# Performance work log

Measured on AMD Instinct MI355X. Metric: run time of the kernel, lower is better.

The kernel has to match this reference:

```python
import jax, jax.numpy as jnp
import numpy as np

HEADS = 16

def setup_inputs() -> dict:
    key = jax.random.key(0)
    k1, k2, k3, k4 = jax.random.split(key, 4)
    B, S, D = 4, 2048, 2048
    x = jax.random.normal(k1, (B, S, D), dtype=jnp.float32)
    Wqkv_w = jax.random.normal(k2, (3 * D, D), dtype=jnp.float32) * (1.0 / np.sqrt(D))
    out_proj_w = jax.random.normal(k3, (D, D), dtype=jnp.float32) * (1.0 / np.sqrt(D))
    attn_bias = jax.random.normal(k4, (1, HEADS, 1, S), dtype=jnp.float32)  # ALiBi-style
    key_padding_mask = jnp.ones((B, S), dtype=jnp.bool_)
    return {"x": x, "Wqkv_w": Wqkv_w, "out_proj_w": out_proj_w,
            "attn_bias": attn_bias, "key_padding_mask": key_padding_mask}

def reference(x, Wqkv_w, out_proj_w, attn_bias, key_padding_mask):
    B, S, D = x.shape
    H = HEADS
    d = D // H
    qkv = jnp.einsum('bsd,ed->bse', x, Wqkv_w)            # [B,S,3D]
    q, k, v = jnp.split(qkv, 3, axis=-1)
    q = q.reshape(B, S, H, d).transpose(0, 2, 1, 3)       # [B,H,S,d]
    k = k.reshape(B, S, H, d).transpose(0, 2, 1, 3)
    v = v.reshape(B, S, H, d).transpose(0, 2, 1, 3)
    scale = 1.0 / np.sqrt(d)
    scores = jnp.einsum('bhqd,bhkd->bhqk', q, k) * scale  # [B,H,S,S]
    scores = scores + attn_bias                           # broadcast over queries
    min_val = jnp.finfo(x.dtype).min
    # key padding mask: (b,1,1,s_k)
    scores = jnp.where(key_padding_mask[:, None, None, :], scores, min_val)
    # causal mask
    causal = jnp.tril(jnp.ones((S, S), dtype=jnp.bool_))
    scores = jnp.where(causal[None, None, :, :], scores, min_val)
    w = jax.nn.softmax(scores, axis=-1)
    out = jnp.einsum('bhqk,bhkd->bhqd', w, v)             # [B,H,S,d]
    out = out.transpose(0, 2, 1, 3).reshape(B, S, D)      # [B,S,D]
    return jnp.einsum('bsd,ed->bse', out, out_proj_w)
```

## Files before the change

### kernel.cpp

```cpp
#include <hip/hip_runtime.h>

typedef float f32x4 __attribute__((ext_vector_type(4)));
typedef __bf16 bf16x8 __attribute__((ext_vector_type(8)));
typedef short s16x8 __attribute__((ext_vector_type(8)));

#define GADDR(p) ((const __attribute__((address_space(1))) void*)(p))
#define LADDR(p) ((__attribute__((address_space(3))) void*)(p))

#define SEQ 2048
#define DH  128
#define NH  16
#define QKV_LD 6144

static __device__ __forceinline__ unsigned short f2bf(float f) {
    unsigned int u = __float_as_uint(f);
    u += 0x7fffu + ((u >> 16) & 1u);
    return (unsigned short)(u >> 16);
}
static __device__ __forceinline__ unsigned short f2bf_fast(float f) {
    return (unsigned short)((__float_as_uint(f) + 0x8000u) >> 16);
}

__global__ __launch_bounds__(256) void cvt_f32_bf16(const float4* __restrict__ in,
                                                    ushort4* __restrict__ out, int n4,
                                                    int n4s, float fac) {
    int stride = gridDim.x * blockDim.x;
    for (int i = blockIdx.x * blockDim.x + threadIdx.x; i < n4; i += stride) {
        float4 v = in[i];
        float f = (i < n4s) ? fac : 1.0f;
        ushort4 o;
        o.x = f2bf(v.x * f); o.y = f2bf(v.y * f); o.z = f2bf(v.z * f); o.w = f2bf(v.w * f);
        out[i] = o;
    }
}

__global__ __launch_bounds__(256) void bias_prep(const float* __restrict__ in,
                                                 float* __restrict__ out, int n) {
    int i = blockIdx.x * blockDim.x + threadIdx.x;
    if (i < n) out[i] = in[i] * 1.4426950408889634f;
}

template<int OUT_BF16>
__global__ __launch_bounds__(512) void gemm8p(const unsigned short* __restrict__ A,
                                              const unsigned short* __restrict__ Bt,
                                              void* __restrict__ Cv, int K, int N) {
    __shared__ __align__(16) unsigned short Als[2][2][8192];
    __shared__ __align__(16) unsigned short Bls[2][2][8192];
    const int tid = threadIdx.x;
    const int w = tid >> 6, l = tid & 63;
    const int lo = l & 15, hi = l >> 4;
    const int wr = w >> 2, wc = w & 3;

    const int nwg = gridDim.x;
    const int cpx = nwg >> 3;
    const int bid = blockIdx.x;
    const int swz = (bid & 7) * cpx + (bid >> 3);
    const int NBN = N >> 8;
    const size_t row0 = (size_t)(swz / NBN) * 256;
    const size_t col0 = (size_t)(swz % NBN) * 256;

    const int srow = w * 16 + (l >> 2);
    const int schunk = (l & 3) ^ ((l >> 3) & 3);
    const int cswz8 = (hi ^ ((lo >> 1) & 3)) * 8;

    const size_t aBase = (row0 + srow) * (size_t)K + schunk * 8;
    const size_t bBase = (col0 + srow) * (size_t)K + schunk * 8;
    const size_t rstep = (size_t)128 * K;

    f32x4 acc[8][4] = {};
    bf16x8 fA[2][4], fB[2][4];

    auto stA = [&](int kt, int kh, int buf) {
        const unsigned short* s = A + aBase + (size_t)kt * 64 + kh * 32;
        unsigned short* lds = &Als[buf][kh][0];
#pragma unroll
        for (int it = 0; it < 2; ++it)
            __builtin_amdgcn_global_load_lds(GADDR(s + it * rstep),
                                             LADDR(lds + it * 4096 + w * 512), 16, 0, 0);
    };
    auto stB = [&](int kt, int kh, int buf) {
        const unsigned short* s = Bt + bBase + (size_t)kt * 64 + kh * 32;
        unsigned short* lds = &Bls[buf][kh][0];
#pragma unroll
        for (int it = 0; it < 2; ++it)
            __builtin_amdgcn_global_load_lds(GADDR(s + it * rstep),
                                             LADDR(lds + it * 4096 + w * 512), 16, 0, 0);
    };

#define LOADA(DST, BUF, KH, MH)                                                            \
    _Pragma("unroll") for (int q = 0; q < 4; ++q)                                          \
        fA[DST][q] = *(const bf16x8*)(&Als[BUF][KH][(wr * 128 + ((MH) * 4 + q) * 16 + lo) * 32 + cswz8]);
#define LOADB(DST, BUF, KH)                                                                \
    _Pragma("unroll") for (int r = 0; r < 4; ++r)                                          \
        fB[DST][r] = *(const bf16x8*)(&Bls[BUF][KH][(wc * 64 + r * 16 + lo) * 32 + cswz8]);

    stA(0, 0, 0); stB(0, 0, 0);
    stA(0, 1, 0); stB(0, 1, 0);
    stA(1, 0, 1); stB(1, 0, 1);
    asm volatile("s_waitcnt vmcnt(8)" ::: "memory");
    __builtin_amdgcn_s_barrier();
    LOADA(0, 0, 0, 0)
    LOADB(0, 0, 0)

    const int NT = K >> 6;
    const int NI = NT >> 1;

#define PHASE(CUR, BCUR, MH, VM, NBUF, NKH, NMH, RB, STAGE_STMT)                           \
    {                                                                                      \
        if (VM) asm volatile("s_waitcnt vmcnt(6)" ::: "memory");                           \
        __builtin_amdgcn_s_barrier();                                                      \
        STAGE_STMT;                                                                        \
        LOADA(1 - (CUR), NBUF, NKH, NMH)                                                   \
        if (RB) { LOADB(1 - (BCUR), NBUF, NKH) }                                           \
        if (RB) asm volatile("s_waitcnt lgkmcnt(8)" ::: "memory");                         \
        else    asm volatile("s_waitcnt lgkmcnt(4)" ::: "memory");                         \
        __builtin_amdgcn_sched_barrier(0);                                                 \
        __builtin_amdgcn_s_setprio(1);                                                     \
        _Pragma("unroll") for (int q = 0; q < 4; ++q)                                      \
            _Pragma("unroll") for (int r = 0; r < 4; ++r)                                  \
                acc[(MH) * 4 + q][r] = __builtin_amdgcn_mfma_f32_16x16x32_bf16(            \
                    fA[CUR][q], fB[BCUR][r], acc[(MH) * 4 + q][r], 0, 0, 0);               \
        __builtin_amdgcn_s_setprio(0);                                                     \
    }

    for (int i = 0; i < NI; ++i) {
        const int t1 = 2 * i + 1;
        int t2 = 2 * i + 2; if (t2 >= NT) t2 = 0;
        int t3 = 2 * i + 3; if (t3 >= NT) t3 = 0;
        PHASE(0, 0, 0, 0, 0, 0, 1, 0, stA(t1, 1, 1))
        PHASE(1, 0, 1, 1, 0, 1, 0, 1, stB(t1, 1, 1))
        PHASE(0, 1, 0, 0, 0, 1, 1, 0, stA(t2, 0, 0))
        PHASE(1, 1, 1, 1, 1, 0, 0, 1, stB(t2, 0, 0))
        PHASE(0, 0, 0, 0, 1, 0, 1, 0, stA(t2, 1, 0))
        PHASE(1, 0, 1, 1, 1, 1, 0, 1, stB(t2, 1, 0))
        PHASE(0, 1, 0, 0, 1, 1, 1, 0, stA(t3, 0, 1))
        PHASE(1, 1, 1, 1, 0, 0, 0, 1, stB(t3, 0, 1))
    }
#undef PHASE
#undef LOADA
#undef LOADB

    asm volatile("s_waitcnt vmcnt(0) lgkmcnt(0)" ::: "memory");

#pragma unroll
    for (int mi = 0; mi < 8; ++mi)
#pragma unroll
        for (int ni = 0; ni < 4; ++ni)
#pragma unroll
            for (int j = 0; j < 4; ++j) {
                size_t r = row0 + wr * 128 + mi * 16 + hi * 4 + j;
                size_t c = col0 + wc * 64 + ni * 16 + lo;
                float v = acc[mi][ni][j];
                if (OUT_BF16) ((unsigned short*)Cv)[r * (size_t)N + c] = f2bf(v);
                else          ((float*)Cv)[r * (size_t)N + c] = v;
            }
}

__global__ __launch_bounds__(256) void transpose_v(const unsigned short* __restrict__ qkv,
                                                   unsigned short* __restrict__ vt) {
    const int st = blockIdx.x;
    const int bh = blockIdx.y;
    const int b = bh >> 4, h = bh & 15;
    const int tid = threadIdx.x;
    __shared__ __align__(16) unsigned short t[64][136];
#pragma unroll
    for (int it = 0; it < 4; ++it) {
        int r = it * 16 + (tid >> 4);
        int c = (tid & 15) * 8;
        *(s16x8*)&t[r][c] =
            *(const s16x8*)(qkv + (size_t)(b * SEQ + st * 64 + r) * QKV_LD + 4096 + h * DH + c);
    }
    __syncthreads();
#pragma unroll
    for (int it = 0; it < 4; ++it) {
        int chunk = it * 256 + tid;
        int d  = chunk >> 3;
        int s0 = (chunk & 7) * 8;
        s16x8 pk;
#pragma unroll
        for (int j = 0; j < 8; ++j) pk[j] = (short)t[s0 + j][d];
        *(s16x8*)(vt + (size_t)(bh * DH + d) * SEQ + st * 64 + s0) = pk;
    }
}

__global__ __launch_bounds__(256) void attn_kernel(const unsigned short* __restrict__ qkv,
                                                   const unsigned short* __restrict__ vt,
                                                   const float* __restrict__ biasp,
                                                   unsigned short* __restrict__ out) {
    const int gx = blockIdx.x & 7;
    const int rr_ = blockIdx.x >> 3;
    const int bh = gx + ((rr_ >> 4) << 3);
    const int pair = rr_ & 15;
    const int b = bh >> 4, h = bh & 15;
    const int tid = threadIdx.x;
    const int w  = tid >> 6, l = tid & 63;
    const int lo = l & 15,  hi = l >> 4;
    const int kx = (lo & 7) << 4;

    __shared__ __align__(16) unsigned short Ks[2][64 * 128];
    __shared__ __align__(16) unsigned short Vs[2][128 * 64];
    __shared__ __align__(16) unsigned short Ps[4][16 * 64];
    __shared__ __align__(16) float BiasLds[2048];

    const int kRowInWave = l >> 4;
    const int kChunkSw_base = l & 15;
    const int vRowInWave = l >> 3;
    const int vChunkSw = (l & 7) ^ ((l >> 3) & 7);

    auto stageKV = [&](int kt, int buf) {
#pragma unroll
        for (int it = 0; it < 4; ++it) {
            int rk = w * 16 + it * 4;
            int kcs = kChunkSw_base ^ ((it * 4 + kRowInWave) & 7);
            __builtin_amdgcn_global_load_lds(
                GADDR(qkv + (size_t)(b * SEQ + kt * 64 + rk + kRowInWave) * QKV_LD
                      + 2048 + h * DH + kcs * 8),
                LADDR(&Ks[buf][rk * 128]), 16, 0, 0);
            int rv = w * 32 + it * 8;
            __builtin_amdgcn_global_load_lds(
                GADDR(vt + (size_t)(bh * DH + rv + vRowInWave) * SEQ
                      + kt * 64 + vChunkSw * 8),
                LADDR(&Vs[buf][rv * 64]), 16, 0, 0);
        }
    };

#pragma unroll
    for (int it = 0; it < 2; ++it)
        __builtin_amdgcn_global_load_lds(
            GADDR(biasp + h * SEQ + w * 512 + it * 256 + l * 4),
            LADDR(&BiasLds[w * 512 + it * 256]), 16, 0, 0);

    for (int rep = 0; rep < 2; ++rep) {
        const int qt = rep ? (31 - pair) : pair;
        const int qbase = qt * 64 + w * 16;

        bf16x8 qf[4];
#pragma unroll
        for (int ds = 0; ds < 4; ++ds)
            qf[ds] = *(const bf16x8*)(qkv + (size_t)(b * SEQ + qbase + lo) * QKV_LD
                                      + h * DH + ds * 32 + hi * 8);

        stageKV(0, 0);

        f32x4 o[8] = {};
        float m[4], lsp[4];
#pragma unroll
        for (int i = 0; i < 4; ++i) { m[i] = -__builtin_inff(); lsp[i] = 0.f; }

        for (int kt = 0; kt <= qt; ++kt) {
            const int cur = kt & 1;
            if (kt < qt) {
                stageKV(kt + 1, cur ^ 1);
                asm volatile("s_waitcnt vmcnt(8)" ::: "memory");
            } else {
                asm volatile("s_waitcnt vmcnt(0)" ::: "memory");
            }
            __builtin_amdgcn_s_barrier();

            float bv[4];
#pragma unroll
            for (int ns = 0; ns < 4; ++ns)
                bv[ns] = BiasLds[kt * 64 + ns * 16 + lo];

            f32x4 sc[4] = {};
            __builtin_amdgcn_s_setprio(1);
#pragma unroll
            for (int ns = 0; ns < 4; ++ns)
#pragma unroll
                for (int ds = 0; ds < 4; ++ds) {
                    bf16x8 kf = *(const bf16x8*)(&Ks[cur][(ns * 16 + lo) * 128
                                 + (((ds * 64 + hi * 16) ^ kx) >> 1)]);
                    sc[ns] = __builtin_amdgcn_mfma_f32_16x16x32_bf16(qf[ds], kf, sc[ns], 0, 0, 0);
                }
            __builtin_amdgcn_s_setprio(0);

            const bool diag = (kt == qt);
#pragma unroll
            for (int i = 0; i < 4; ++i) {
                float s[4];
#pragma unroll
                for (int ns = 0; ns < 4; ++ns)
                    s[ns] = sc[ns][i] + bv[ns];
                if (diag) {
                    int qg = qbase + hi * 4 + i;
#pragma unroll
                    for (int ns = 0; ns < 4; ++ns)
                        if (kt * 64 + ns * 16 + lo > qg) s[ns] = -__builtin_inff();
                }
                float rm = fmaxf(fmaxf(s[0], s[1]), fmaxf(s[2], s[3]));
#pragma unroll
                for (int off = 1; off <= 8; off <<= 1)
                    rm = fmaxf(rm, __shfl_xor(rm, off, 64));
                if (rm > m[i] + 8.0f) {
                    float corr = __builtin_amdgcn_exp2f(m[i] - rm);
                    m[i] = rm;
                    lsp[i] *= corr;
#pragma unroll
                    for (int nd = 0; nd < 8; ++nd) o[nd][i] *= corr;
                }
                int prow = hi * 4 + i;
                int pbase = prow * 64;
                int pxor = (prow & 7) << 4;
                float psum = 0.f;
#pragma unroll
                for (int ns = 0; ns < 4; ++ns) {
                    float p = __builtin_amdgcn_exp2f(s[ns] - m[i]);
                    psum += p;
                    Ps[w][pbase + (((ns * 32 + lo * 2) ^ pxor) >> 1)] = f2bf_fast(p);
                }
                lsp[i] += psum;
            }

            __builtin_amdgcn_s_setprio(1);
#pragma unroll
            for (int ks = 0; ks < 2; ++ks) {
                bf16x8 pf = *(const bf16x8*)(&Ps[w][lo * 64
                             + (((ks * 64 + hi * 16) ^ kx) >> 1)]);
#pragma unroll
                for (int nd = 0; nd < 8; ++nd) {
                    bf16x8 vf = *(const bf16x8*)(&Vs[cur][(nd * 16 + lo) * 64
                                 + (((ks * 64 + hi * 16) ^ kx) >> 1)]);
                    o[nd] = __builtin_amdgcn_mfma_f32_16x16x32_bf16(pf, vf, o[nd], 0, 0, 0);
                }
            }
            __builtin_amdgcn_s_setprio(0);
            __builtin_amdgcn_s_barrier();
        }

#pragma unroll
        for (int i = 0; i < 4; ++i) {
            float rs = lsp[i];
#pragma unroll
            for (int off = 1; off <= 8; off <<= 1)
                rs += __shfl_xor(rs, off, 64);
            float inv = 1.0f / rs;
            size_t row = (size_t)(b * SEQ + qbase + hi * 4 + i) * 2048 + h * DH;
#pragma unroll
            for (int nd = 0; nd < 8; ++nd)
                out[row + nd * 16 + lo] = f2bf(o[nd][i] * inv);
        }
    }
}

extern "C" void kernel_launch(void* const* d_in, const int* in_sizes, int n_in,
                              void* d_out, int out_size, void* d_ws, size_t ws_size,
                              hipStream_t stream) {
    const float* x    = (const float*)d_in[0];
    const float* wqkv = (const float*)d_in[1];
    const float* wout = (const float*)d_in[2];
    const float* bias = (const float*)d_in[3];

    char* ws = (char*)d_ws;
    unsigned short* xb    = (unsigned short*)(ws);
    unsigned short* wqkvb = (unsigned short*)(ws + 33554432);
    unsigned short* woutb = (unsigned short*)(ws + 58720256);
    unsigned short* qkv   = (unsigned short*)(ws + 67108864);
    unsigned short* vt    = (unsigned short*)(ws + 167772160);
    unsigned short* attn  = xb;
    float* biasp = (float*)(ws + 33554432);

    const float QS = 0.08838834764831845f * 1.4426950408889634f;

    cvt_f32_bf16<<<1024, 256, 0, stream>>>((const float4*)x,    (ushort4*)xb,
                                           16777216 / 4, 0, 1.0f);
    cvt_f32_bf16<<<1024, 256, 0, stream>>>((const float4*)wqkv, (ushort4*)wqkvb,
                                           12582912 / 4, 4194304 / 4, QS);
    cvt_f32_bf16<<<1024, 256, 0, stream>>>((const float4*)wout, (ushort4*)woutb,
                                           4194304 / 4, 0, 1.0f);

    gemm8p<1><<<768, 512, 0, stream>>>(xb, wqkvb, qkv, 2048, 6144);

    bias_prep<<<128, 256, 0, stream>>>(bias, biasp, NH * SEQ);

    transpose_v<<<dim3(32, 64), 256, 0, stream>>>(qkv, vt);

    attn_kernel<<<1024, 256, 0, stream>>>(qkv, vt, biasp, attn);

    gemm8p<0><<<256, 512, 0, stream>>>(attn, woutb, (float*)d_out, 2048, 2048);
}
```

Measured before the change: 486.4 us.

## Drop LDS-to-register double buffering in GEMM main loop

Replaces the double-buffered fragment registers (fA/fB with two slots) with single-buffered fragments that are loaded from LDS and consumed within the same phase. A second barrier per phase is added so LDS buffers are not overwritten while still in use, and lgkmcnt waits become full drains. This frees VGPRs and simplifies the schedule, but it loses the overlap of LDS reads with MFMA compute and doubles the barrier count.

```diff
diff --git a/kernel.cpp b/kernel.cpp
--- a/kernel.cpp
+++ b/kernel.cpp
@@ -68,7 +68,7 @@
     const size_t rstep = (size_t)128 * K;
 
     f32x4 acc[8][4] = {};
-    bf16x8 fA[2][4], fB[2][4];
+    bf16x8 fA[4], fB[4];
 
     auto stA = [&](int kt, int kh, int buf) {
         const unsigned short* s = A + aBase + (size_t)kt * 64 + kh * 32;
@@ -87,54 +87,52 @@
                                              LADDR(lds + it * 4096 + w * 512), 16, 0, 0);
     };
 
-#define LOADA(DST, BUF, KH, MH)                                                            \
+#define LOADA(BUF, KH, MH)                                                                 \
     _Pragma("unroll") for (int q = 0; q < 4; ++q)                                          \
-        fA[DST][q] = *(const bf16x8*)(&Als[BUF][KH][(wr * 128 + ((MH) * 4 + q) * 16 + lo) * 32 + cswz8]);
-#define LOADB(DST, BUF, KH)                                                                \
+        fA[q] = *(const bf16x8*)(&Als[BUF][KH][(wr * 128 + ((MH) * 4 + q) * 16 + lo) * 32 + cswz8]);
+#define LOADB(BUF, KH)                                                                     \
     _Pragma("unroll") for (int r = 0; r < 4; ++r)                                          \
-        fB[DST][r] = *(const bf16x8*)(&Bls[BUF][KH][(wc * 64 + r * 16 + lo) * 32 + cswz8]);
+        fB[r] = *(const bf16x8*)(&Bls[BUF][KH][(wc * 64 + r * 16 + lo) * 32 + cswz8]);
 
     stA(0, 0, 0); stB(0, 0, 0);
     stA(0, 1, 0); stB(0, 1, 0);
     stA(1, 0, 1); stB(1, 0, 1);
-    asm volatile("s_waitcnt vmcnt(8)" ::: "memory");
+    asm volatile("s_waitcnt vmcnt(4)" ::: "memory");
     __builtin_amdgcn_s_barrier();
-    LOADA(0, 0, 0, 0)
-    LOADB(0, 0, 0)
 
     const int NT = K >> 6;
     const int NI = NT >> 1;
 
-#define PHASE(CUR, BCUR, MH, VM, NBUF, NKH, NMH, RB, STAGE_STMT)                           \
+#define PHASE(BUF, KH, MH, RDB, VM, STAGE_STMT)                                            \
     {                                                                                      \
-        if (VM) asm volatile("s_waitcnt vmcnt(6)" ::: "memory");                           \
+        if (VM) asm volatile("s_waitcnt vmcnt(4)" ::: "memory");                           \
+        LOADA(BUF, KH, MH)                                                                 \
+        if (RDB) { LOADB(BUF, KH) }                                                        \
+        STAGE_STMT;                                                                        \
         __builtin_amdgcn_s_barrier();                                                      \
-        STAGE_STMT;                                                                        \
-        LOADA(1 - (CUR), NBUF, NKH, NMH)                                                   \
-        if (RB) { LOADB(1 - (BCUR), NBUF, NKH) }                                           \
-        if (RB) asm volatile("s_waitcnt lgkmcnt(8)" ::: "memory");                         \
-        else    asm volatile("s_waitcnt lgkmcnt(4)" ::: "memory");                         \
+        asm volatile("s_waitcnt lgkmcnt(0)" ::: "memory");                                 \
         __builtin_amdgcn_sched_barrier(0);                                                 \
         __builtin_amdgcn_s_setprio(1);                                                     \
         _Pragma("unroll") for (int q = 0; q < 4; ++q)                                      \
             _Pragma("unroll") for (int r = 0; r < 4; ++r)                                  \
                 acc[(MH) * 4 + q][r] = __builtin_amdgcn_mfma_f32_16x16x32_bf16(            \
-                    fA[CUR][q], fB[BCUR][r], acc[(MH) * 4 + q][r], 0, 0, 0);               \
+                    fA[q], fB[r], acc[(MH) * 4 + q][r], 0, 0, 0);                          \
         __builtin_amdgcn_s_setprio(0);                                                     \
+        __builtin_amdgcn_s_barrier();                                                      \
     }
 
     for (int i = 0; i < NI; ++i) {
         const int t1 = 2 * i + 1;
         int t2 = 2 * i + 2; if (t2 >= NT) t2 = 0;
         int t3 = 2 * i + 3; if (t3 >= NT) t3 = 0;
-        PHASE(0, 0, 0, 0, 0, 0, 1, 0, stA(t1, 1, 1))
-        PHASE(1, 0, 1, 1, 0, 1, 0, 1, stB(t1, 1, 1))
-        PHASE(0, 1, 0, 0, 0, 1, 1, 0, stA(t2, 0, 0))
-        PHASE(1, 1, 1, 1, 1, 0, 0, 1, stB(t2, 0, 0))
-        PHASE(0, 0, 0, 0, 1, 0, 1, 0, stA(t2, 1, 0))
-        PHASE(1, 0, 1, 1, 1, 1, 0, 1, stB(t2, 1, 0))
-        PHASE(0, 1, 0, 0, 1, 1, 1, 0, stA(t3, 0, 1))
-        PHASE(1, 1, 1, 1, 0, 0, 0, 1, stB(t3, 0, 1))
+        PHASE(0, 0, 0, 1, 0, stA(t1, 1, 1))
+        PHASE(0, 0, 1, 0, 0, stB(t1, 1, 1))
+        PHASE(0, 1, 0, 1, 0, stA(t2, 0, 0))
+        PHASE(0, 1, 1, 0, 1, stB(t2, 0, 0))
+        PHASE(1, 0, 0, 1, 0, stA(t2, 1, 0))
+        PHASE(1, 0, 1, 0, 0, stB(t2, 1, 0))
+        PHASE(1, 1, 0, 1, 0, stA(t3, 0, 1))
+        PHASE(1, 1, 1, 0, 1, stB(t3, 0, 1))
     }
 #undef PHASE
 #undef LOADA
```

Measured after the change: 485.0 us. Within noise of the previous version (-0.3%).
